# Optimization experiments

Measured on AMD Instinct MI355X. Metric: run time of the kernel, lower is better.

## Reference

```python
import jax, jax.numpy as jnp
import numpy as np

B, C, N, M = 8, 128, 2048, 512

def setup_inputs() -> dict:
    key = jax.random.key(0)
    k1, k2, k3, k4 = jax.random.split(key, 4)
    scale = 1.0 / np.sqrt(C)
    x = jax.random.normal(k1, (B, C, N), dtype=jnp.float32)
    # conv1d with kernel size 1 and no bias == channel-mixing matmul, weight [C_out, C_in]
    Wq = jax.random.normal(k2, (C, C), dtype=jnp.float32) * scale
    Wk = jax.random.normal(k3, (C, C), dtype=jnp.float32) * scale
    Wv = jax.random.normal(k4, (C, C), dtype=jnp.float32) * scale
    return {"x": x, "Wq": Wq, "Wk": Wk, "Wv": Wv, "npts_ds": M}

def reference(x, Wq, Wk, Wv, npts_ds):
    # q,k,v: [B,C,N] via 1x1 conv == einsum over input channels
    q = jnp.einsum('oc,bcn->bon', Wq, x)
    k = jnp.einsum('oc,bcn->bon', Wk, x)
    v = jnp.einsum('oc,bcn->bon', Wv, x)
    # energy: [B,N,N] = q^T k (contract channel dim)
    energy = jnp.einsum('bcn,bcm->bnm', q, k)
    scale_factor = jnp.sqrt(jnp.asarray(q.shape[-2], dtype=energy.dtype))  # sqrt(C)
    attention = jax.nn.softmax(energy / scale_factor, axis=-1)  # [B,N,N]
    selection = jnp.sum(attention, axis=-2)  # [B,N] column sums
    _, idx = jax.lax.top_k(selection, npts_ds)  # [B,M]
    # gather selected attention rows: [B,M,N]
    scores = jnp.take_along_axis(attention, idx[:, :, None], axis=1)
    # weighted sum of values: [B,M,C]
    out = jnp.einsum('bmn,bcn->bcm', scores, v)  # [B,C,M]
    return out
```

## Files before the change

### kernel.cpp

```cpp
#include <hip/hip_runtime.h>
#include <math.h>

namespace {
constexpr int B = 8, C = 128, N = 2048, M = 512;
constexpr int NSPLIT = 8;
constexpr int MBLK = 16;
constexpr float INV_SQRT_C = 0.08838834764831845f;
}

typedef __attribute__((ext_vector_type(8))) short short8;
typedef __attribute__((ext_vector_type(16))) float f32x16;
typedef unsigned short ushort_t;
typedef unsigned int u32;

__device__ inline ushort_t f2bf(float f) {
  union { float f; u32 u; } a; a.f = f;
  u32 r = a.u + 0x7fffu + ((a.u >> 16) & 1u);
  return (ushort_t)(r >> 16);
}
__device__ inline float bf2f(ushort_t h) {
  union { u32 u; float f; } a; a.u = ((u32)h) << 16; return a.f;
}

__global__ __launch_bounds__(256) void qkv_kernel(
    const float* __restrict__ x, const float* __restrict__ Wq,
    const float* __restrict__ Wk, const float* __restrict__ Wv,
    ushort_t* __restrict__ split, ushort_t* __restrict__ vbf) {
  const size_t TERM = (size_t)B * N * C;
  int kc = blockIdx.x;
  int o0 = kc * 8;
  int n = blockIdx.y * 256 + threadIdx.x;
  int b = blockIdx.z;
  const float* xb = x + (size_t)b * C * N + n;
  float aq[8] = {}, ak[8] = {}, av[8] = {};
  #pragma unroll 4
  for (int c = 0; c < C; ++c) {
    float xv = xb[(size_t)c * N];
    #pragma unroll
    for (int j = 0; j < 8; ++j) {
      aq[j] = fmaf(Wq[(o0 + j) * C + c], xv, aq[j]);
      ak[j] = fmaf(Wk[(o0 + j) * C + c], xv, ak[j]);
      av[j] = fmaf(Wv[(o0 + j) * C + c], xv, av[j]);
    }
  }
  #pragma unroll
  for (int j = 0; j < 8; ++j)
    vbf[((size_t)b * C + o0 + j) * N + n] = f2bf(av[j]);
  size_t rowoff = ((size_t)b * 16 + kc) * (size_t)N * 8 + (size_t)n * 8;
  #pragma unroll
  for (int tt = 0; tt < 3; ++tt) {
    short8 qv, kv;
    #pragma unroll
    for (int j = 0; j < 8; ++j) {
      ushort_t h = f2bf(aq[j]); qv[j] = (short)h; aq[j] -= bf2f(h);
      h = f2bf(ak[j]);          kv[j] = (short)h; ak[j] -= bf2f(h);
    }
    *(short8*)&split[tt * TERM + rowoff]       = qv;
    *(short8*)&split[(3 + tt) * TERM + rowoff] = kv;
  }
}

__global__ __launch_bounds__(256) void energy_kernel(
    const ushort_t* __restrict__ split,
    float* __restrict__ Ae, float* __restrict__ rowpart) {
  __shared__ float red[128][64];
  __shared__ float red2[128][2];
  const size_t TERM = (size_t)B * N * C;
  const size_t ROW8 = (size_t)N * 8;
  int t = threadIdx.x;
  int lane = t & 63, w = t >> 6;
  int wn = w & 1, wm = w >> 1;
  int lin = blockIdx.y * 16 + blockIdx.x;
  int st = lin >> 4, wi = lin & 15;
  int mb = (st & 3) * 4 + (wi & 3);
  int nb = (st >> 2) * 4 + (wi >> 2);
  int m0 = mb * 128, n0 = nb * 128, b = blockIdx.z;
  int lr = lane & 31, lq = lane >> 5;
  size_t kbase = ((size_t)b * 16 + lq) * ROW8;
  const ushort_t* Abase = split + kbase + (size_t)(n0 + wn * 64 + lr) * 8;
  const ushort_t* Bbase = split + 3 * TERM + kbase + (size_t)(m0 + wm * 64 + lr) * 8;
  f32x16 acc[2][2] = {};
  #pragma unroll
  for (int s = 0; s < 8; ++s) {
    size_t so = (size_t)s * 2 * ROW8;
    short8 aT[3][2], bT[3][2];
    #pragma unroll
    for (int tt = 0; tt < 3; ++tt)
      #pragma unroll
      for (int i = 0; i < 2; ++i) {
        aT[tt][i] = *(const short8*)(Abase + tt * TERM + so + i * 256);
        bT[tt][i] = *(const short8*)(Bbase + tt * TERM + so + i * 256);
      }
    #pragma unroll
    for (int mt = 0; mt < 2; ++mt)
      #pragma unroll
      for (int nt = 0; nt < 2; ++nt) {
        acc[mt][nt] = __builtin_amdgcn_mfma_f32_32x32x16_bf16(aT[0][mt], bT[0][nt], acc[mt][nt], 0, 0, 0);
        acc[mt][nt] = __builtin_amdgcn_mfma_f32_32x32x16_bf16(aT[1][mt], bT[0][nt], acc[mt][nt], 0, 0, 0);
        acc[mt][nt] = __builtin_amdgcn_mfma_f32_32x32x16_bf16(aT[0][mt], bT[1][nt], acc[mt][nt], 0, 0, 0);
        acc[mt][nt] = __builtin_amdgcn_mfma_f32_32x32x16_bf16(aT[2][mt], bT[0][nt], acc[mt][nt], 0, 0, 0);
        acc[mt][nt] = __builtin_amdgcn_mfma_f32_32x32x16_bf16(aT[1][mt], bT[1][nt], acc[mt][nt], 0, 0, 0);
        acc[mt][nt] = __builtin_amdgcn_mfma_f32_32x32x16_bf16(aT[0][mt], bT[2][nt], acc[mt][nt], 0, 0, 0);
      }
  }
  int lc = lr;
  #pragma unroll
  for (int mt = 0; mt < 2; ++mt) {
    #pragma unroll
    for (int reg = 0; reg < 16; ++reg) {
      int row = (reg & 3) + 8 * (reg >> 2) + 4 * lq;
      int rloc = wn * 64 + mt * 32 + row;
      float e0 = expf(acc[mt][0][reg] * INV_SQRT_C);
      float e1 = expf(acc[mt][1][reg] * INV_SQRT_C);
      float* pA = Ae + ((size_t)b * N + n0 + rloc) * N + m0 + wm * 64 + lc;
      pA[0] = e0; pA[32] = e1;
      red[rloc][wm * 32 + lc] = e0 + e1;
    }
  }
  __syncthreads();
  {
    int row = t >> 1, h = t & 1;
    float ssum = 0.f;
    #pragma unroll
    for (int j0 = 0; j0 < 32; ++j0) {
      int j = (j0 + (t & 31)) & 31;
      ssum += red[row][h * 32 + j];
    }
    red2[row][h] = ssum;
  }
  __syncthreads();
  if (t < 128)
    rowpart[(size_t)mb * (B * N) + b * N + n0 + t] = red2[t][0] + red2[t][1];
}

__global__ __launch_bounds__(256) void colsum_kernel(
    const float* __restrict__ Ae, const float* __restrict__ rowpart,
    float* __restrict__ selpart) {
  __shared__ float sinv[256];
  int t = threadIdx.x;
  int m = blockIdx.x * 256 + t;
  int nch = blockIdx.y, b = blockIdx.z;
  int n0 = nch * (N / 8);
  {
    int n = n0 + t;
    float s = 0.f;
    #pragma unroll
    for (int sl = 0; sl < MBLK; ++sl)
      s += rowpart[(size_t)sl * (B * N) + b * N + n];
    sinv[t] = 1.0f / s;
  }
  __syncthreads();
  const float* Ab = Ae + (size_t)b * N * N;
  float acc = 0.f;
  #pragma unroll 8
  for (int n = n0; n < n0 + N / 8; ++n)
    acc = fmaf(Ab[(size_t)n * N + m], sinv[n - n0], acc);
  selpart[(size_t)nch * (B * N) + b * N + m] = acc;
}

__global__ __launch_bounds__(256) void topk_kernel(
    const float* __restrict__ selpart, int* __restrict__ idx) {
  __shared__ float s[N];
  __shared__ int rsum[64][4];
  int b = blockIdx.y;
  int t = threadIdx.x;
  for (int i = t; i < N; i += 256) {
    float v_ = 0.f;
    #pragma unroll
    for (int nch = 0; nch < 8; ++nch)
      v_ += selpart[(size_t)nch * (B * N) + b * N + i];
    s[i] = v_;
  }
  __syncthreads();
  int i = blockIdx.x * 64 + (t & 63);
  int jc = t >> 6;
  float val = s[i];
  int r = 0;
  for (int j = jc * 512; j < jc * 512 + 512; ++j) {
    float sj = s[j];
    r += (sj > val || (sj == val && j < i)) ? 1 : 0;
  }
  rsum[t & 63][jc] = r;
  __syncthreads();
  if (t < 64) {
    int rank = rsum[t][0] + rsum[t][1] + rsum[t][2] + rsum[t][3];
    if (rank < M) idx[b * M + rank] = blockIdx.x * 64 + t;
  }
}

__global__ __launch_bounds__(256) void out_kernel(
    const float* __restrict__ Ae, const float* __restrict__ rowpart,
    const ushort_t* __restrict__ vbf, const int* __restrict__ idx,
    float* __restrict__ part) {
  __shared__ ushort_t sc[64][72];
  __shared__ ushort_t vt[128][72];
  __shared__ int ridx[64];
  __shared__ float rinv[64];
  int t = threadIdx.x;
  int m0 = blockIdx.x * 64;
  int ns = blockIdx.y;
  int b = blockIdx.z;
  if (t < 64) {
    int r = idx[b * M + m0 + t];
    ridx[t] = r;
    float s = 0.f;
    #pragma unroll
    for (int sl = 0; sl < MBLK; ++sl)
      s += rowpart[(size_t)sl * (B * N) + b * N + r];
    rinv[t] = 1.0f / s;
  }
  __syncthreads();
  int lane = t & 63, w = t >> 6;
  int wc = w & 1, wm = w >> 1;
  int lr = lane & 31, lq = lane >> 5;
  f32x16 acc[2] = {};
  int nbeg = ns * (N / NSPLIT);
  for (int kb = 0; kb < N / NSPLIT; kb += 64) {
    __syncthreads();
    #pragma unroll
    for (int it = 0; it < 16; ++it) {
      int ii = it * 256 + t;
      int r = ii >> 6, cn = ii & 63;
      float sv = Ae[((size_t)b * N + ridx[r]) * N + nbeg + kb + cn] * rinv[r];
      sc[r][cn] = f2bf(sv);
    }
    #pragma unroll
    for (int it = 0; it < 4; ++it) {
      int u = it * 256 + t;
      int r = u >> 3, seg = u & 7;
      *(short8*)&vt[r][seg * 8] =
          *(const short8*)&vbf[((size_t)b * C + r) * N + nbeg + kb + seg * 8];
    }
    __syncthreads();
    #pragma unroll
    for (int ks = 0; ks < 4; ++ks) {
      short8 bf_ = *(const short8*)&sc[wm * 32 + lr][ks * 16 + lq * 8];
      #pragma unroll
      for (int ct = 0; ct < 2; ++ct) {
        short8 af = *(const short8*)&vt[wc * 64 + ct * 32 + lr][ks * 16 + lq * 8];
        acc[ct] = __builtin_amdgcn_mfma_f32_32x32x16_bf16(af, bf_, acc[ct], 0, 0, 0);
      }
    }
  }
  float* pb = part + ((size_t)ns * B + b) * C * M;
  #pragma unroll
  for (int ct = 0; ct < 2; ++ct) {
    #pragma unroll
    for (int reg = 0; reg < 16; ++reg) {
      int crow = wc * 64 + ct * 32 + (reg & 3) + 8 * (reg >> 2) + 4 * lq;
      pb[(size_t)crow * M + m0 + wm * 32 + lr] = acc[ct][reg];
    }
  }
}

__global__ __launch_bounds__(256) void reduce_kernel(
    const float* __restrict__ part, float* __restrict__ out) {
  int i = (blockIdx.x * 256 + threadIdx.x) * 4;
  float4 a = make_float4(0.f, 0.f, 0.f, 0.f);
  #pragma unroll
  for (int ns = 0; ns < NSPLIT; ++ns) {
    float4 p = *(const float4*)&part[(size_t)ns * (B * C * M) + i];
    a.x += p.x; a.y += p.y; a.z += p.z; a.w += p.w;
  }
  *(float4*)&out[i] = a;
}

extern "C" void kernel_launch(void* const* d_in, const int* in_sizes, int n_in,
                              void* d_out, int out_size, void* d_ws, size_t ws_size,
                              hipStream_t stream) {
  const float* x  = (const float*)d_in[0];
  const float* Wq = (const float*)d_in[1];
  const float* Wk = (const float*)d_in[2];
  const float* Wv = (const float*)d_in[3];
  float* out = (float*)d_out;

  const size_t TSZ = (size_t)B * N * C;
  ushort_t* split = (ushort_t*)d_ws;
  ushort_t* vbf   = split + 6 * TSZ;
  float* Ae       = (float*)(vbf + TSZ);
  float* rowpart  = Ae + (size_t)B * N * N;
  float* selpart  = rowpart + (size_t)MBLK * B * N;
  int*   idx      = (int*)(selpart + (size_t)8 * B * N);
  float* part     = (float*)split;

  qkv_kernel<<<dim3(16, N / 256, B), 256, 0, stream>>>(x, Wq, Wk, Wv, split, vbf);
  energy_kernel<<<dim3(N / 128, N / 128, B), 256, 0, stream>>>(split, Ae, rowpart);
  colsum_kernel<<<dim3(N / 256, 8, B), 256, 0, stream>>>(Ae, rowpart, selpart);
  topk_kernel<<<dim3(N / 64, B), 256, 0, stream>>>(selpart, idx);
  out_kernel<<<dim3(M / 64, NSPLIT, B), 256, 0, stream>>>(Ae, rowpart, vbf, idx, part);
  reduce_kernel<<<dim3(B * C * M / 1024), 256, 0, stream>>>(part, out);
}
```

Before: 236.7 us.

## Stage energy GEMM operands through double-buffered LDS via direct global-to-LDS loads

The energy kernel now loads the split bf16 Q/K tiles into a double-buffered shared-memory staging area with global_load_lds, one 16-byte chunk per thread. It then reads MFMA operands from LDS instead of issuing per-wave global loads. The next k-slice is prefetched while the current one runs on MFMA, and each tile is fetched once per block rather than once per wave. The staging buffer shares LDS with the reduction arrays through a union. In exchange it adds a barrier every k-step and relies on the async LDS loads being complete at each sync.

```diff
diff --git a/kernel.cpp b/kernel.cpp
--- a/kernel.cpp
+++ b/kernel.cpp
@@ -20,6 +20,12 @@
 }
 __device__ inline float bf2f(ushort_t h) {
   union { u32 u; float f; } a; a.u = ((u32)h) << 16; return a.f;
+}
+
+__device__ __forceinline__ void gl_lds16(const ushort_t* g, ushort_t* l) {
+  __builtin_amdgcn_global_load_lds(
+      (const __attribute__((address_space(1))) unsigned int*)g,
+      (__attribute__((address_space(3))) unsigned int*)l, 16, 0, 0);
 }
 
 __global__ __launch_bounds__(256) void qkv_kernel(
@@ -63,8 +69,10 @@
 __global__ __launch_bounds__(256) void energy_kernel(
     const ushort_t* __restrict__ split,
     float* __restrict__ Ae, float* __restrict__ rowpart) {
-  __shared__ float red[128][64];
-  __shared__ float red2[128][2];
+  __shared__ __align__(16) union {
+    ushort_t stg[2][12288];
+    struct { float red[128][64]; float red2[128][2]; } r;
+  } sm;
   const size_t TERM = (size_t)B * N * C;
   const size_t ROW8 = (size_t)N * 8;
   int t = threadIdx.x;
@@ -76,20 +84,40 @@
   int nb = (st >> 2) * 4 + (wi >> 2);
   int m0 = mb * 128, n0 = nb * 128, b = blockIdx.z;
   int lr = lane & 31, lq = lane >> 5;
-  size_t kbase = ((size_t)b * 16 + lq) * ROW8;
-  const ushort_t* Abase = split + kbase + (size_t)(n0 + wn * 64 + lr) * 8;
-  const ushort_t* Bbase = split + 3 * TERM + kbase + (size_t)(m0 + wm * 64 + lr) * 8;
+
+  const ushort_t* gA = split + (size_t)b * 16 * ROW8
+                     + (size_t)(t >> 7) * ROW8 + ((size_t)n0 + (t & 127)) * 8;
+  const ushort_t* gB = split + 3 * TERM + (size_t)b * 16 * ROW8
+                     + (size_t)(t >> 7) * ROW8 + ((size_t)m0 + (t & 127)) * 8;
+
   f32x16 acc[2][2] = {};
   #pragma unroll
+  for (int tt = 0; tt < 3; ++tt) {
+    gl_lds16(gA + (size_t)tt * TERM, &sm.stg[0][tt * 2048 + t * 8]);
+    gl_lds16(gB + (size_t)tt * TERM, &sm.stg[0][(3 + tt) * 2048 + t * 8]);
+  }
+  __syncthreads();
+
+  const int aoff = (lq * 128 + wn * 64 + lr) * 8;
+  const int boff = (lq * 128 + wm * 64 + lr) * 8;
+  #pragma unroll
   for (int s = 0; s < 8; ++s) {
-    size_t so = (size_t)s * 2 * ROW8;
+    const int cur = s & 1;
+    if (s < 7) {
+      size_t so = (size_t)(2 * (s + 1)) * ROW8;
+      #pragma unroll
+      for (int tt = 0; tt < 3; ++tt) {
+        gl_lds16(gA + (size_t)tt * TERM + so, &sm.stg[cur ^ 1][tt * 2048 + t * 8]);
+        gl_lds16(gB + (size_t)tt * TERM + so, &sm.stg[cur ^ 1][(3 + tt) * 2048 + t * 8]);
+      }
+    }
     short8 aT[3][2], bT[3][2];
     #pragma unroll
     for (int tt = 0; tt < 3; ++tt)
       #pragma unroll
       for (int i = 0; i < 2; ++i) {
-        aT[tt][i] = *(const short8*)(Abase + tt * TERM + so + i * 256);
-        bT[tt][i] = *(const short8*)(Bbase + tt * TERM + so + i * 256);
+        aT[tt][i] = *(const short8*)&sm.stg[cur][tt * 2048 + aoff + i * 256];
+        bT[tt][i] = *(const short8*)&sm.stg[cur][(3 + tt) * 2048 + boff + i * 256];
       }
     #pragma unroll
     for (int mt = 0; mt < 2; ++mt)
@@ -102,6 +130,7 @@
         acc[mt][nt] = __builtin_amdgcn_mfma_f32_32x32x16_bf16(aT[1][mt], bT[1][nt], acc[mt][nt], 0, 0, 0);
         acc[mt][nt] = __builtin_amdgcn_mfma_f32_32x32x16_bf16(aT[0][mt], bT[2][nt], acc[mt][nt], 0, 0, 0);
       }
+    __syncthreads();
   }
   int lc = lr;
   #pragma unroll
@@ -114,7 +143,7 @@
       float e1 = expf(acc[mt][1][reg] * INV_SQRT_C);
       float* pA = Ae + ((size_t)b * N + n0 + rloc) * N + m0 + wm * 64 + lc;
       pA[0] = e0; pA[32] = e1;
-      red[rloc][wm * 32 + lc] = e0 + e1;
+      sm.r.red[rloc][wm * 32 + lc] = e0 + e1;
     }
   }
   __syncthreads();
@@ -124,13 +153,13 @@
     #pragma unroll
     for (int j0 = 0; j0 < 32; ++j0) {
       int j = (j0 + (t & 31)) & 31;
-      ssum += red[row][h * 32 + j];
-    }
-    red2[row][h] = ssum;
+      ssum += sm.r.red[row][h * 32 + j];
+    }
+    sm.r.red2[row][h] = ssum;
   }
   __syncthreads();
   if (t < 128)
-    rowpart[(size_t)mb * (B * N) + b * N + n0 + t] = red2[t][0] + red2[t][1];
+    rowpart[(size_t)mb * (B * N) + b * N + n0 + t] = sm.r.red2[t][0] + sm.r.red2[t][1];
 }
 
 __global__ __launch_bounds__(256) void colsum_kernel(
```

Measured after the change: 229.3 us. 3.2% less time.
